# Optimization experiments

Measured on AMD Instinct MI355X. Metric: run time of the kernel, lower is better.

## Reference

```python
import jax, jax.numpy as jnp
import numpy as np

NEG_SLOPE = 0.2  # LeakyReLU slope from the torch module


def setup_inputs() -> dict:
    key = jax.random.key(0)
    k1, k2, k3 = jax.random.split(key, 3)
    B, N, IN = 32, 512, 256
    H, D = 8, 32  # out_dim=256, concat=True -> head_dim = 256 // 8
    x = jax.random.normal(k1, (B, N, IN), dtype=jnp.float32)
    # nn.Linear(in_dim, H*D, bias=False).weight has shape (H*D, in_dim)
    W = jax.random.normal(k2, (H * D, IN), dtype=jnp.float32) * (1.0 / np.sqrt(IN))
    # xavier_uniform on (1, H, 2D)
    limit = float(np.sqrt(6.0 / (H + 2 * D)))
    attn = jax.random.uniform(k3, (1, H, 2 * D), dtype=jnp.float32, minval=-limit, maxval=limit)
    return {"x": x, "W": W, "attn": attn}


def reference(x, W, attn):
    # x: (B, N, IN); W: (H*D, IN); attn: (1, H, 2D)
    B, N, _ = x.shape
    H = attn.shape[1]
    D = attn.shape[2] // 2
    Wx = (x @ W.T).reshape(B, N, H, D)  # (B, N, H, D)
    # Additive attention decomposes: e[b,i,j,h] = leaky(s_src[b,i,h] + s_tgt[b,j,h]).
    # (src = Wx broadcast over j, tgt = Wx broadcast over i; cat*attn sums split in two.)
    a_src = attn[0, :, :D]  # (H, D)
    a_tgt = attn[0, :, D:]  # (H, D)
    s_src = jnp.einsum('bnhd,hd->bnh', Wx, a_src)
    s_tgt = jnp.einsum('bnhd,hd->bnh', Wx, a_tgt)
    e = jax.nn.leaky_relu(s_src[:, :, None, :] + s_tgt[:, None, :, :], NEG_SLOPE)  # (B,N,N,H)
    a = jax.nn.softmax(e, axis=2)  # softmax over source nodes j
    # dropout p=0 (eval mode) -> identity
    out = jnp.einsum('bijh,bjhd->bihd', a, Wx)  # (B, N, H, D)
    out = out.reshape(B, N, H * D)  # concat=True
    return jax.nn.elu(out)
```

## Files before the change

kernel.cpp:

```cpp
#include <hip/hip_runtime.h>
#include <math.h>

#define NEG_SLOPE 0.2f
#define LOG2E 1.44269504088896f

#if __has_builtin(__builtin_amdgcn_exp2f)
#define EXP2F __builtin_amdgcn_exp2f
#else
#define EXP2F exp2f
#endif

typedef _Float16 f16x8 __attribute__((ext_vector_type(8)));
typedef __fp16 h16x2 __attribute__((ext_vector_type(2)));
typedef float f32x4 __attribute__((ext_vector_type(4)));
typedef float f32x2 __attribute__((ext_vector_type(2)));

union PK8 { uint4 u4; _Float16 h[8]; f16x8 v; h16x2 p[4]; };
union PKH { h16x2 v; unsigned int u; unsigned short s[2]; };
union PK1 { unsigned short u; _Float16 h; };

#define WN_CHUNKS (256 * 256 / 8)

__global__ __launch_bounds__(256) void cvt_w(const float* __restrict__ W,
                                             unsigned short* __restrict__ wf) {
    int idx = blockIdx.x * 256 + threadIdx.x;
    if (idx >= WN_CHUNKS) return;
    const float* src = W + (size_t)idx * 8;
    float4 v0 = *(const float4*)(src);
    float4 v1 = *(const float4*)(src + 4);
    PK8 p;
    p.p[0] = __builtin_amdgcn_cvt_pkrtz(v0.x, v0.y);
    p.p[1] = __builtin_amdgcn_cvt_pkrtz(v0.z, v0.w);
    p.p[2] = __builtin_amdgcn_cvt_pkrtz(v1.x, v1.y);
    p.p[3] = __builtin_amdgcn_cvt_pkrtz(v1.z, v1.w);
    *(uint4*)(wf + (size_t)idx * 8) = p.u4;
}

__global__ __launch_bounds__(256) void gemm_wxt(const float* __restrict__ x,
                                                const unsigned short* __restrict__ wf,
                                                unsigned short* __restrict__ wxtg) {
    __shared__ __align__(16) unsigned short xs[64 * 64];
    __shared__ __align__(16) unsigned short pool[128 * 64];
    unsigned short* ws = pool;
    unsigned short* tb = pool;

    const int tid = threadIdx.x;
    const int bid = blockIdx.x;
    const int m0 = (bid & 255) * 64;
    const int n0 = (bid >> 8) * 128;
    const int w = tid >> 6, l = tid & 63;
    const int q = l >> 4, ln = l & 15;
    const int iw = (w & 1) * 32, nw = (w >> 1) * 64;

    f32x4 acc[2][4];
    #pragma unroll
    for (int g = 0; g < 2; ++g)
        #pragma unroll
        for (int t = 0; t < 4; ++t) acc[g][t] = (f32x4){0.f, 0.f, 0.f, 0.f};

    for (int kc = 0; kc < 256; kc += 64) {
        __syncthreads();
        {
            const int i = tid >> 2, kq = tid & 3;
            const float* src = x + (size_t)(m0 + i) * 256 + kc + kq * 16;
            float4 v0 = *(const float4*)(src + 0);
            float4 v1 = *(const float4*)(src + 4);
            float4 v2 = *(const float4*)(src + 8);
            float4 v3 = *(const float4*)(src + 12);
            PK8 p0, p1;
            p0.p[0] = __builtin_amdgcn_cvt_pkrtz(v0.x, v0.y);
            p0.p[1] = __builtin_amdgcn_cvt_pkrtz(v0.z, v0.w);
            p0.p[2] = __builtin_amdgcn_cvt_pkrtz(v1.x, v1.y);
            p0.p[3] = __builtin_amdgcn_cvt_pkrtz(v1.z, v1.w);
            p1.p[0] = __builtin_amdgcn_cvt_pkrtz(v2.x, v2.y);
            p1.p[1] = __builtin_amdgcn_cvt_pkrtz(v2.z, v2.w);
            p1.p[2] = __builtin_amdgcn_cvt_pkrtz(v3.x, v3.y);
            p1.p[3] = __builtin_amdgcn_cvt_pkrtz(v3.z, v3.w);
            int b0 = i * 128 + kq * 32;
            *(uint4*)((char*)xs + (b0 ^ ((i & 7) << 4))) = p0.u4;
            *(uint4*)((char*)xs + ((b0 + 16) ^ ((i & 7) << 4))) = p1.u4;
        }
        #pragma unroll
        for (int p = 0; p < 4; ++p) {
            int idx = p * 256 + tid;
            int n = idx >> 3, c = idx & 7;
            uint4 v = *(const uint4*)(wf + (size_t)(n0 + n) * 256 + kc + c * 8);
            *(uint4*)((char*)ws + ((n * 128 + c * 16) ^ ((n & 7) << 4))) = v;
        }
        __syncthreads();

        #pragma unroll
        for (int ks = 0; ks < 2; ++ks) {
            const int kb = ks * 64 + q * 16;
            f16x8 af[2];
            #pragma unroll
            for (int g = 0; g < 2; ++g) {
                int row = iw + g * 16 + ln;
                uint4 raw = *(const uint4*)((const char*)xs +
                            ((row * 128 + kb) ^ ((row & 7) << 4)));
                PK8 pk; pk.u4 = raw;
                af[g] = pk.v;
            }
            #pragma unroll
            for (int t = 0; t < 4; ++t) {
                int n = nw + t * 16 + ln;
                uint4 raw = *(const uint4*)((const char*)ws +
                            ((n * 128 + kb) ^ ((n & 7) << 4)));
                PK8 pk; pk.u4 = raw;
                f16x8 bf = pk.v;
                acc[0][t] = __builtin_amdgcn_mfma_f32_16x16x32_f16(af[0], bf, acc[0][t], 0, 0, 0);
                acc[1][t] = __builtin_amdgcn_mfma_f32_16x16x32_f16(af[1], bf, acc[1][t], 0, 0, 0);
            }
        }
    }

    __syncthreads();
    #pragma unroll
    for (int g = 0; g < 2; ++g)
        #pragma unroll
        for (int t = 0; t < 4; ++t)
            #pragma unroll
            for (int r = 0; r < 4; ++r) {
                int n  = nw + t * 16 + ln;
                int jl = iw + g * 16 + q * 4 + r;
                PK1 hv; hv.h = (_Float16)acc[g][t][r];
                *(unsigned short*)((char*)tb + ((n * 128 + jl * 2) ^ ((n & 7) << 4))) = hv.u;
            }
    __syncthreads();
    {
        const int b = m0 >> 9, j0 = m0 & 511;
        #pragma unroll
        for (int p = 0; p < 4; ++p) {
            int idx = p * 256 + tid;
            int n = idx >> 3, c = idx & 7;
            uint4 v = *(const uint4*)((const char*)tb + ((n * 128 + c * 16) ^ ((n & 7) << 4)));
            int nn = n0 + n;
            *(uint4*)(wxtg + ((size_t)(b * 256 + nn) * 512 + j0 + c * 8)) = v;
        }
    }
}

__global__ __launch_bounds__(512, 4) void gat_attn(const unsigned short* __restrict__ wxtg,
                                                   const float* __restrict__ attn,
                                                   float* __restrict__ out) {
    __shared__ __align__(16) unsigned short wxt[32 * 512];
    __shared__ float stf[512];
    __shared__ float ssrc[512];
    __shared__ float red_s[8];

    const int bid = blockIdx.x;
    const int bh = bid & 255, half = bid >> 8;
    const int b = bh >> 3, h = bh & 7;
    const int tid = threadIdx.x;
    const int w = tid >> 6, l = tid & 63;
    const int q = l >> 4, ln = l & 15;

    {
        const unsigned short* src = wxtg + (size_t)bh * 32 * 512;
        const int d = tid >> 4, cs = tid & 15;
        #pragma unroll
        for (int p = 0; p < 4; ++p) {
            int c = p * 16 + cs;
            uint4 v = *(const uint4*)(src + d * 512 + c * 8);
            *(uint4*)((char*)wxt + ((d * 1024 + c * 16) ^ ((d & 7) << 4))) = v;
        }
    }
    __syncthreads();

    {
        const int j = tid;
        float ss = 0.f, st = 0.f;
        #pragma unroll
        for (int d = 0; d < 32; ++d) {
            PK1 hv;
            hv.u = *(const unsigned short*)((const char*)wxt +
                    ((d * 1024 + j * 2) ^ ((d & 7) << 4)));
            float v = (float)hv.h;
            ss += v * attn[h * 64 + d];
            st += v * attn[h * 64 + 32 + d];
        }
        ssrc[j] = ss * LOG2E;
        float stv = st * LOG2E;
        stf[j] = stv;
        float m = stv;
        #pragma unroll
        for (int off = 32; off > 0; off >>= 1)
            m = fmaxf(m, __shfl_xor(m, off));
        if (l == 0) red_s[w] = m;
    }
    __syncthreads();
    float maxtK = red_s[0];
    #pragma unroll
    for (int ww = 1; ww < 8; ++ww) maxtK = fmaxf(maxtK, red_s[ww]);

    const int ibase = half * 256 + w * 32;
    float ciK[2], miK[2];
    #pragma unroll
    for (int g = 0; g < 2; ++g) {
        float cc = ssrc[ibase + g * 16 + ln];
        float cm = cc + maxtK;
        miK[g] = fmaxf(cm, NEG_SLOPE * cm);
        ciK[g] = cc;
    }

    f32x4 acc[2][2];
    #pragma unroll
    for (int g = 0; g < 2; ++g) {
        acc[g][0] = (f32x4){0.f, 0.f, 0.f, 0.f};
        acc[g][1] = (f32x4){0.f, 0.f, 0.f, 0.f};
    }
    f32x2 pdv[2] = {(f32x2){0.f, 0.f}, (f32x2){0.f, 0.f}};

    #pragma unroll 2
    for (int kk = 0; kk < 16; ++kk) {
        const int j0 = kk * 32 + q * 8;
        f32x2 stp[4];
        {
            float4 s0 = *(const float4*)(stf + j0);
            float4 s1 = *(const float4*)(stf + j0 + 4);
            stp[0] = (f32x2){s0.x, s0.y};
            stp[1] = (f32x2){s0.z, s0.w};
            stp[2] = (f32x2){s1.x, s1.y};
            stp[3] = (f32x2){s1.z, s1.w};
        }

        f16x8 bf[2];
        #pragma unroll
        for (int dt = 0; dt < 2; ++dt) {
            int d = dt * 16 + ln;
            int bb = d * 1024 + kk * 64 + q * 16;
            uint4 raw = *(const uint4*)((const char*)wxt + (bb ^ ((d & 7) << 4)));
            PK8 pk; pk.u4 = raw;
            bf[dt] = pk.v;
        }

        #pragma unroll
        for (int g = 0; g < 2; ++g) {
            const f32x2 ci2 = (f32x2){ciK[g], ciK[g]};
            const f32x2 mi2 = (f32x2){miK[g], miK[g]};
            PK8 pa;
            #pragma unroll
            for (int pr = 0; pr < 4; ++pr) {
                f32x2 e  = ci2 + stp[pr];
                f32x2 a1 = e - mi2;
                f32x2 a2 = (f32x2){NEG_SLOPE, NEG_SLOPE} * e - mi2;
                float m0 = fmaxf(a1.x, a2.x);
                float m1 = fmaxf(a1.y, a2.y);
                float p0 = EXP2F(m0);
                float p1 = EXP2F(m1);
                pdv[g] += (f32x2){p0, p1};
                pa.p[pr] = __builtin_amdgcn_cvt_pkrtz(p0, p1);
            }
            acc[g][0] = __builtin_amdgcn_mfma_f32_16x16x32_f16(pa.v, bf[0], acc[g][0], 0, 0, 0);
            acc[g][1] = __builtin_amdgcn_mfma_f32_16x16x32_f16(pa.v, bf[1], acc[g][1], 0, 0, 0);
        }
    }

    float inv[2];
    #pragma unroll
    for (int g = 0; g < 2; ++g) {
        float s = pdv[g].x + pdv[g].y;
        s += __shfl_xor(s, 16);
        s += __shfl_xor(s, 32);
        inv[g] = 1.f / s;
    }
    #pragma unroll
    for (int g = 0; g < 2; ++g)
        #pragma unroll
        for (int dt = 0; dt < 2; ++dt)
            #pragma unroll
            for (int r = 0; r < 4; ++r) {
                int row = q * 4 + r;
                float dn = __shfl(inv[g], row);
                float o = acc[g][dt][r] * dn;
                o = o > 0.f ? o : (__expf(o) - 1.f);
                size_t i = (size_t)(b * 512 + ibase + g * 16 + row);
                out[i * 256 + h * 32 + dt * 16 + ln] = o;
            }
}

extern "C" void kernel_launch(void* const* d_in, const int* in_sizes, int n_in,
                              void* d_out, int out_size, void* d_ws, size_t ws_size,
                              hipStream_t stream) {
    const float* x    = (const float*)d_in[0];
    const float* W    = (const float*)d_in[1];
    const float* attn = (const float*)d_in[2];
    float* out = (float*)d_out;

    unsigned short* wf   = (unsigned short*)d_ws;
    unsigned short* wxtg = wf + 256 * 256;

    cvt_w<<<WN_CHUNKS / 256, 256, 0, stream>>>(W, wf);
    gemm_wxt<<<512, 256, 0, stream>>>(x, wf, wxtg);
    gat_attn<<<512, 512, 0, stream>>>(wxtg, attn, out);
}
```

Baseline: 41.89 us.

## Halve per-block work in GEMM and attention kernels to double grid size

```diff
diff --git a/kernel.cpp b/kernel.cpp
--- a/kernel.cpp
+++ b/kernel.cpp
@@ -16,7 +16,6 @@
 typedef float f32x2 __attribute__((ext_vector_type(2)));
 
 union PK8 { uint4 u4; _Float16 h[8]; f16x8 v; h16x2 p[4]; };
-union PKH { h16x2 v; unsigned int u; unsigned short s[2]; };
 union PK1 { unsigned short u; _Float16 h; };
 
 #define WN_CHUNKS (256 * 256 / 8)
@@ -40,23 +39,23 @@
                                                 const unsigned short* __restrict__ wf,
                                                 unsigned short* __restrict__ wxtg) {
     __shared__ __align__(16) unsigned short xs[64 * 64];
-    __shared__ __align__(16) unsigned short pool[128 * 64];
+    __shared__ __align__(16) unsigned short pool[64 * 64];
     unsigned short* ws = pool;
     unsigned short* tb = pool;
 
     const int tid = threadIdx.x;
     const int bid = blockIdx.x;
     const int m0 = (bid & 255) * 64;
-    const int n0 = (bid >> 8) * 128;
+    const int n0 = (bid >> 8) * 64;
     const int w = tid >> 6, l = tid & 63;
     const int q = l >> 4, ln = l & 15;
-    const int iw = (w & 1) * 32, nw = (w >> 1) * 64;
-
-    f32x4 acc[2][4];
+    const int iw = (w & 1) * 32, nw = (w >> 1) * 32;
+
+    f32x4 acc[2][2];
     #pragma unroll
     for (int g = 0; g < 2; ++g)
         #pragma unroll
-        for (int t = 0; t < 4; ++t) acc[g][t] = (f32x4){0.f, 0.f, 0.f, 0.f};
+        for (int t = 0; t < 2; ++t) acc[g][t] = (f32x4){0.f, 0.f, 0.f, 0.f};
 
     for (int kc = 0; kc < 256; kc += 64) {
         __syncthreads();
@@ -81,7 +80,7 @@
             *(uint4*)((char*)xs + ((b0 + 16) ^ ((i & 7) << 4))) = p1.u4;
         }
         #pragma unroll
-        for (int p = 0; p < 4; ++p) {
+        for (int p = 0; p < 2; ++p) {
             int idx = p * 256 + tid;
             int n = idx >> 3, c = idx & 7;
             uint4 v = *(const uint4*)(wf + (size_t)(n0 + n) * 256 + kc + c * 8);
@@ -102,7 +101,7 @@
                 af[g] = pk.v;
             }
             #pragma unroll
-            for (int t = 0; t < 4; ++t) {
+            for (int t = 0; t < 2; ++t) {
                 int n = nw + t * 16 + ln;
                 uint4 raw = *(const uint4*)((const char*)ws +
                             ((n * 128 + kb) ^ ((n & 7) << 4)));
@@ -118,7 +117,7 @@
     #pragma unroll
     for (int g = 0; g < 2; ++g)
         #pragma unroll
-        for (int t = 0; t < 4; ++t)
+        for (int t = 0; t < 2; ++t)
             #pragma unroll
             for (int r = 0; r < 4; ++r) {
                 int n  = nw + t * 16 + ln;
@@ -130,7 +129,7 @@
     {
         const int b = m0 >> 9, j0 = m0 & 511;
         #pragma unroll
-        for (int p = 0; p < 4; ++p) {
+        for (int p = 0; p < 2; ++p) {
             int idx = p * 256 + tid;
             int n = idx >> 3, c = idx & 7;
             uint4 v = *(const uint4*)((const char*)tb + ((n * 128 + c * 16) ^ ((n & 7) << 4)));
@@ -140,7 +139,7 @@
     }
 }
 
-__global__ __launch_bounds__(512, 4) void gat_attn(const unsigned short* __restrict__ wxtg,
+__global__ __launch_bounds__(512, 8) void gat_attn(const unsigned short* __restrict__ wxtg,
                                                    const float* __restrict__ attn,
                                                    float* __restrict__ out) {
     __shared__ __align__(16) unsigned short wxt[32 * 512];
@@ -149,7 +148,7 @@
     __shared__ float red_s[8];
 
     const int bid = blockIdx.x;
-    const int bh = bid & 255, half = bid >> 8;
+    const int bh = bid & 255, quart = bid >> 8;
     const int b = bh >> 3, h = bh & 7;
     const int tid = threadIdx.x;
     const int w = tid >> 6, l = tid & 63;
@@ -193,25 +192,19 @@
     #pragma unroll
     for (int ww = 1; ww < 8; ++ww) maxtK = fmaxf(maxtK, red_s[ww]);
 
-    const int ibase = half * 256 + w * 32;
-    float ciK[2], miK[2];
-    #pragma unroll
-    for (int g = 0; g < 2; ++g) {
-        float cc = ssrc[ibase + g * 16 + ln];
+    const int ibase = quart * 128 + w * 16;
+    float ciK, miK;
+    {
+        float cc = ssrc[ibase + ln];
         float cm = cc + maxtK;
-        miK[g] = fmaxf(cm, NEG_SLOPE * cm);
-        ciK[g] = cc;
-    }
-
-    f32x4 acc[2][2];
-    #pragma unroll
-    for (int g = 0; g < 2; ++g) {
-        acc[g][0] = (f32x4){0.f, 0.f, 0.f, 0.f};
-        acc[g][1] = (f32x4){0.f, 0.f, 0.f, 0.f};
-    }
-    f32x2 pdv[2] = {(f32x2){0.f, 0.f}, (f32x2){0.f, 0.f}};
-
-    #pragma unroll 2
+        miK = fmaxf(cm, NEG_SLOPE * cm);
+        ciK = cc;
+    }
+
+    f32x4 acc0 = (f32x4){0.f, 0.f, 0.f, 0.f};
+    f32x4 acc1 = (f32x4){0.f, 0.f, 0.f, 0.f};
+    f32x2 pdv = (f32x2){0.f, 0.f};
+
     for (int kk = 0; kk < 16; ++kk) {
         const int j0 = kk * 32 + q * 8;
         f32x2 stp[4];
@@ -234,49 +227,45 @@
             bf[dt] = pk.v;
         }
 
-        #pragma unroll
-        for (int g = 0; g < 2; ++g) {
-            const f32x2 ci2 = (f32x2){ciK[g], ciK[g]};
-            const f32x2 mi2 = (f32x2){miK[g], miK[g]};
-            PK8 pa;
-            #pragma unroll
-            for (int pr = 0; pr < 4; ++pr) {
-                f32x2 e  = ci2 + stp[pr];
-                f32x2 a1 = e - mi2;
-                f32x2 a2 = (f32x2){NEG_SLOPE, NEG_SLOPE} * e - mi2;
-                float m0 = fmaxf(a1.x, a2.x);
-                float m1 = fmaxf(a1.y, a2.y);
-                float p0 = EXP2F(m0);
-                float p1 = EXP2F(m1);
-                pdv[g] += (f32x2){p0, p1};
-                pa.p[pr] = __builtin_amdgcn_cvt_pkrtz(p0, p1);
-            }
-            acc[g][0] = __builtin_amdgcn_mfma_f32_16x16x32_f16(pa.v, bf[0], acc[g][0], 0, 0, 0);
-            acc[g][1] = __builtin_amdgcn_mfma_f32_16x16x32_f16(pa.v, bf[1], acc[g][1], 0, 0, 0);
-        }
-    }
-
-    float inv[2];
-    #pragma unroll
-    for (int g = 0; g < 2; ++g) {
-        float s = pdv[g].x + pdv[g].y;
+        const f32x2 ci2 = (f32x2){ciK, ciK};
+        const f32x2 mi2 = (f32x2){miK, miK};
+        PK8 pa;
+        #pragma unroll
+        for (int pr = 0; pr < 4; ++pr) {
+            f32x2 e  = ci2 + stp[pr];
+            f32x2 a1 = e - mi2;
+            f32x2 a2 = (f32x2){NEG_SLOPE, NEG_SLOPE} * e - mi2;
+            float m0 = fmaxf(a1.x, a2.x);
+            float m1 = fmaxf(a1.y, a2.y);
+            float p0 = EXP2F(m0);
+            float p1 = EXP2F(m1);
+            pdv += (f32x2){p0, p1};
+            pa.p[pr] = __builtin_amdgcn_cvt_pkrtz(p0, p1);
+        }
+        acc0 = __builtin_amdgcn_mfma_f32_16x16x32_f16(pa.v, bf[0], acc0, 0, 0, 0);
+        acc1 = __builtin_amdgcn_mfma_f32_16x16x32_f16(pa.v, bf[1], acc1, 0, 0, 0);
+    }
+
+    float inv;
+    {
+        float s = pdv.x + pdv.y;
         s += __shfl_xor(s, 16);
         s += __shfl_xor(s, 32);
-        inv[g] = 1.f / s;
-    }
-    #pragma unroll
-    for (int g = 0; g < 2; ++g)
-        #pragma unroll
-        for (int dt = 0; dt < 2; ++dt)
-            #pragma unroll
-            for (int r = 0; r < 4; ++r) {
-                int row = q * 4 + r;
-                float dn = __shfl(inv[g], row);
-                float o = acc[g][dt][r] * dn;
-                o = o > 0.f ? o : (__expf(o) - 1.f);
-                size_t i = (size_t)(b * 512 + ibase + g * 16 + row);
-                out[i * 256 + h * 32 + dt * 16 + ln] = o;
-            }
+        inv = 1.f / s;
+    }
+    #pragma unroll
+    for (int dt = 0; dt < 2; ++dt) {
+        f32x4 a = dt ? acc1 : acc0;
+        #pragma unroll
+        for (int r = 0; r < 4; ++r) {
+            int row = q * 4 + r;
+            float dn = __shfl(inv, row);
+            float o = a[r] * dn;
+            o = o > 0.f ? o : (__expf(o) - 1.f);
+            size_t i = (size_t)(b * 512 + ibase + row);
+            out[i * 256 + h * 32 + dt * 16 + ln] = o;
+        }
+    }
 }
 
 extern "C" void kernel_launch(void* const* d_in, const int* in_sizes, int n_in,
@@ -291,6 +280,6 @@
     unsigned short* wxtg = wf + 256 * 256;
 
     cvt_w<<<WN_CHUNKS / 256, 256, 0, stream>>>(W, wf);
-    gemm_wxt<<<512, 256, 0, stream>>>(x, wf, wxtg);
-    gat_attn<<<512, 512, 0, stream>>>(wxtg, attn, out);
-}
+    gemm_wxt<<<1024, 256, 0, stream>>>(x, wf, wxtg);
+    gat_attn<<<1024, 512, 0, stream>>>(wxtg, attn, out);
+}
```

New measurement: 41.30 us. Within noise of the previous version (-1.4%).

## Fuse attention score projections into GEMM epilogue and read Wx directly from global

Applied to the files above, without the earlier changes.

```diff
diff --git a/kernel.cpp b/kernel.cpp
--- a/kernel.cpp
+++ b/kernel.cpp
@@ -16,7 +16,6 @@
 typedef float f32x2 __attribute__((ext_vector_type(2)));
 
 union PK8 { uint4 u4; _Float16 h[8]; f16x8 v; h16x2 p[4]; };
-union PKH { h16x2 v; unsigned int u; unsigned short s[2]; };
 union PK1 { unsigned short u; _Float16 h; };
 
 #define WN_CHUNKS (256 * 256 / 8)
@@ -38,25 +37,28 @@
 
 __global__ __launch_bounds__(256) void gemm_wxt(const float* __restrict__ x,
                                                 const unsigned short* __restrict__ wf,
-                                                unsigned short* __restrict__ wxtg) {
+                                                const float* __restrict__ attn,
+                                                unsigned short* __restrict__ wxtg,
+                                                float* __restrict__ s_src,
+                                                float* __restrict__ s_tgt) {
     __shared__ __align__(16) unsigned short xs[64 * 64];
-    __shared__ __align__(16) unsigned short pool[128 * 64];
+    __shared__ __align__(16) unsigned short pool[64 * 64];
     unsigned short* ws = pool;
     unsigned short* tb = pool;
 
     const int tid = threadIdx.x;
     const int bid = blockIdx.x;
     const int m0 = (bid & 255) * 64;
-    const int n0 = (bid >> 8) * 128;
+    const int n0 = (bid >> 8) * 64;
     const int w = tid >> 6, l = tid & 63;
     const int q = l >> 4, ln = l & 15;
-    const int iw = (w & 1) * 32, nw = (w >> 1) * 64;
-
-    f32x4 acc[2][4];
+    const int iw = (w & 1) * 32, nw = (w >> 1) * 32;
+
+    f32x4 acc[2][2];
     #pragma unroll
     for (int g = 0; g < 2; ++g)
         #pragma unroll
-        for (int t = 0; t < 4; ++t) acc[g][t] = (f32x4){0.f, 0.f, 0.f, 0.f};
+        for (int t = 0; t < 2; ++t) acc[g][t] = (f32x4){0.f, 0.f, 0.f, 0.f};
 
     for (int kc = 0; kc < 256; kc += 64) {
         __syncthreads();
@@ -81,7 +83,7 @@
             *(uint4*)((char*)xs + ((b0 + 16) ^ ((i & 7) << 4))) = p1.u4;
         }
         #pragma unroll
-        for (int p = 0; p < 4; ++p) {
+        for (int p = 0; p < 2; ++p) {
             int idx = p * 256 + tid;
             int n = idx >> 3, c = idx & 7;
             uint4 v = *(const uint4*)(wf + (size_t)(n0 + n) * 256 + kc + c * 8);
@@ -102,7 +104,7 @@
                 af[g] = pk.v;
             }
             #pragma unroll
-            for (int t = 0; t < 4; ++t) {
+            for (int t = 0; t < 2; ++t) {
                 int n = nw + t * 16 + ln;
                 uint4 raw = *(const uint4*)((const char*)ws +
                             ((n * 128 + kb) ^ ((n & 7) << 4)));
@@ -114,11 +116,40 @@
         }
     }
 
+    {
+        const int h = (n0 + nw) >> 5;
+        float avs[2], avt[2];
+        #pragma unroll
+        for (int t = 0; t < 2; ++t) {
+            avs[t] = attn[h * 64 + t * 16 + ln];
+            avt[t] = attn[h * 64 + 32 + t * 16 + ln];
+        }
+        const int bb = m0 >> 9;
+        const int jbase = (m0 & 511) + iw;
+        const int bh = bb * 8 + h;
+        #pragma unroll
+        for (int g = 0; g < 2; ++g)
+            #pragma unroll
+            for (int r = 0; r < 4; ++r) {
+                float ps = acc[g][0][r] * avs[0] + acc[g][1][r] * avs[1];
+                float pt = acc[g][0][r] * avt[0] + acc[g][1][r] * avt[1];
+                ps += __shfl_xor(ps, 1); ps += __shfl_xor(ps, 2);
+                ps += __shfl_xor(ps, 4); ps += __shfl_xor(ps, 8);
+                pt += __shfl_xor(pt, 1); pt += __shfl_xor(pt, 2);
+                pt += __shfl_xor(pt, 4); pt += __shfl_xor(pt, 8);
+                if (ln == 0) {
+                    int j = jbase + g * 16 + q * 4 + r;
+                    s_src[bh * 512 + j] = ps;
+                    s_tgt[bh * 512 + j] = pt;
+                }
+            }
+    }
+
     __syncthreads();
     #pragma unroll
     for (int g = 0; g < 2; ++g)
         #pragma unroll
-        for (int t = 0; t < 4; ++t)
+        for (int t = 0; t < 2; ++t)
             #pragma unroll
             for (int r = 0; r < 4; ++r) {
                 int n  = nw + t * 16 + ln;
@@ -128,24 +159,23 @@
             }
     __syncthreads();
     {
-        const int b = m0 >> 9, j0 = m0 & 511;
-        #pragma unroll
-        for (int p = 0; p < 4; ++p) {
+        const int bb = m0 >> 9, j0 = m0 & 511;
+        #pragma unroll
+        for (int p = 0; p < 2; ++p) {
             int idx = p * 256 + tid;
             int n = idx >> 3, c = idx & 7;
             uint4 v = *(const uint4*)((const char*)tb + ((n * 128 + c * 16) ^ ((n & 7) << 4)));
             int nn = n0 + n;
-            *(uint4*)(wxtg + ((size_t)(b * 256 + nn) * 512 + j0 + c * 8)) = v;
+            *(uint4*)(wxtg + ((size_t)(bb * 256 + nn) * 512 + j0 + c * 8)) = v;
         }
     }
 }
 
 __global__ __launch_bounds__(512, 4) void gat_attn(const unsigned short* __restrict__ wxtg,
-                                                   const float* __restrict__ attn,
+                                                   const float* __restrict__ s_src,
+                                                   const float* __restrict__ s_tgt,
                                                    float* __restrict__ out) {
-    __shared__ __align__(16) unsigned short wxt[32 * 512];
     __shared__ float stf[512];
-    __shared__ float ssrc[512];
     __shared__ float red_s[8];
 
     const int bid = blockIdx.x;
@@ -156,32 +186,8 @@
     const int q = l >> 4, ln = l & 15;
 
     {
-        const unsigned short* src = wxtg + (size_t)bh * 32 * 512;
-        const int d = tid >> 4, cs = tid & 15;
-        #pragma unroll
-        for (int p = 0; p < 4; ++p) {
-            int c = p * 16 + cs;
-            uint4 v = *(const uint4*)(src + d * 512 + c * 8);
-            *(uint4*)((char*)wxt + ((d * 1024 + c * 16) ^ ((d & 7) << 4))) = v;
-        }
-    }
-    __syncthreads();
-
-    {
-        const int j = tid;
-        float ss = 0.f, st = 0.f;
-        #pragma unroll
-        for (int d = 0; d < 32; ++d) {
-            PK1 hv;
-            hv.u = *(const unsigned short*)((const char*)wxt +
-                    ((d * 1024 + j * 2) ^ ((d & 7) << 4)));
-            float v = (float)hv.h;
-            ss += v * attn[h * 64 + d];
-            st += v * attn[h * 64 + 32 + d];
-        }
-        ssrc[j] = ss * LOG2E;
-        float stv = st * LOG2E;
-        stf[j] = stv;
+        float stv = s_tgt[bh * 512 + tid] * LOG2E;
+        stf[tid] = stv;
         float m = stv;
         #pragma unroll
         for (int off = 32; off > 0; off >>= 1)
@@ -197,12 +203,15 @@
     float ciK[2], miK[2];
     #pragma unroll
     for (int g = 0; g < 2; ++g) {
-        float cc = ssrc[ibase + g * 16 + ln];
+        float cc = s_src[bh * 512 + ibase + g * 16 + ln] * LOG2E;
         float cm = cc + maxtK;
         miK[g] = fmaxf(cm, NEG_SLOPE * cm);
         ciK[g] = cc;
     }
 
+    const unsigned short* pb0 = wxtg + (size_t)bh * 16384 + ln * 512 + q * 8;
+    const unsigned short* pb1 = pb0 + 16 * 512;
+
     f32x4 acc[2][2];
     #pragma unroll
     for (int g = 0; g < 2; ++g) {
@@ -213,6 +222,14 @@
 
     #pragma unroll 2
     for (int kk = 0; kk < 16; ++kk) {
+        f16x8 bf[2];
+        {
+            PK8 pk0, pk1;
+            pk0.u4 = *(const uint4*)(pb0 + kk * 32);
+            pk1.u4 = *(const uint4*)(pb1 + kk * 32);
+            bf[0] = pk0.v;
+            bf[1] = pk1.v;
+        }
         const int j0 = kk * 32 + q * 8;
         f32x2 stp[4];
         {
@@ -222,16 +239,6 @@
             stp[1] = (f32x2){s0.z, s0.w};
             stp[2] = (f32x2){s1.x, s1.y};
             stp[3] = (f32x2){s1.z, s1.w};
-        }
-
-        f16x8 bf[2];
-        #pragma unroll
-        for (int dt = 0; dt < 2; ++dt) {
-            int d = dt * 16 + ln;
-            int bb = d * 1024 + kk * 64 + q * 16;
-            uint4 raw = *(const uint4*)((const char*)wxt + (bb ^ ((d & 7) << 4)));
-            PK8 pk; pk.u4 = raw;
-            bf[dt] = pk.v;
         }
 
         #pragma unroll
@@ -289,8 +296,10 @@
 
     unsigned short* wf   = (unsigned short*)d_ws;
     unsigned short* wxtg = wf + 256 * 256;
+    float* s_src = (float*)(wxtg + (size_t)256 * 32 * 512);
+    float* s_tgt = s_src + 256 * 512;
 
     cvt_w<<<WN_CHUNKS / 256, 256, 0, stream>>>(W, wf);
-    gemm_wxt<<<512, 256, 0, stream>>>(x, wf, wxtg);
-    gat_attn<<<512, 512, 0, stream>>>(wxtg, attn, out);
+    gemm_wxt<<<1024, 256, 0, stream>>>(x, wf, attn, wxtg, s_src, s_tgt);
+    gat_attn<<<512, 512, 0, stream>>>(wxtg, s_src, s_tgt, out);
 }
```

After: 43.27 us. 1.03x slower.
